# Performance work log

Measured on AMD Instinct MI355X. Metric: run time of the kernel, lower is better.

## Reference

```python
import jax, jax.numpy as jnp
import numpy as np

N, C_IN, H, W = 32, 3, 224, 224
C_OUT, K, STRIDE, PAD = 64, 3, 1, 1


def setup_inputs() -> dict:
    key = jax.random.key(0)
    k1, k2 = jax.random.split(key)
    x = jax.random.normal(k1, (N, C_IN, H, W), dtype=jnp.float32)
    weight = jax.random.normal(k2, (C_OUT, C_IN, K, K), dtype=jnp.float32)
    bias = jnp.zeros((C_OUT,), dtype=jnp.float32)
    return {"x": x, "weight": weight, "bias": bias}


def reference(x, weight, bias):
    # Equivalent to the manual im2col + GEMM: a standard 2D convolution
    # (cross-correlation, as the torch code slides the raw kernel).
    out = jax.lax.conv_general_dilated(
        x, weight,
        window_strides=(STRIDE, STRIDE),
        padding=[(PAD, PAD), (PAD, PAD)],
        dimension_numbers=("NCHW", "OIHW", "NCHW"),
    )
    return out + bias[None, :, None, None]
```

## Files before the change

kernel.cpp:

```cpp
#include <hip/hip_runtime.h>


#define N_IMG 32
#define C_IN 3
#define H_ 224
#define W_ 224
#define C_OUT 64
#define NPIX (H_ * W_)
#define W4 (W_ / 4)
#define STRIPS (NPIX / 4)
#define COB 16

__global__ __launch_bounds__(256) void conv3x3_v2(
    const float* __restrict__ x,
    const float* __restrict__ wgt,
    const float* __restrict__ bias,
    float* __restrict__ out)
{
    const int s  = blockIdx.x * 256 + threadIdx.x;
    const int n  = blockIdx.y;
    const int cb = blockIdx.z * COB;
    const int h  = s / W4;
    const int w4 = (s - h * W4) * 4;

    float win[C_IN][3][6];
    const float* xn = x + (size_t)n * C_IN * NPIX;
#pragma unroll
    for (int ci = 0; ci < C_IN; ++ci) {
#pragma unroll
        for (int r = 0; r < 3; ++r) {
            const int hh = h + r - 1;
            const bool hok = (unsigned)hh < (unsigned)H_;
            const float* row = xn + ci * NPIX + hh * W_;
            if (hok) {
                const float4 m = *reinterpret_cast<const float4*>(row + w4);
                win[ci][r][1] = m.x; win[ci][r][2] = m.y;
                win[ci][r][3] = m.z; win[ci][r][4] = m.w;
                win[ci][r][0] = (w4 > 0)      ? row[w4 - 1] : 0.0f;
                win[ci][r][5] = (w4 + 4 < W_) ? row[w4 + 4] : 0.0f;
            } else {
#pragma unroll
                for (int c = 0; c < 6; ++c) win[ci][r][c] = 0.0f;
            }
        }
    }

    float* outp = out + ((size_t)n * C_OUT + cb) * NPIX + h * W_ + w4;
#pragma unroll
    for (int i = 0; i < COB; ++i) {
        const float* wp = wgt + (size_t)(cb + i) * 27;
        const float b  = bias[cb + i];
        float a0 = b, a1 = b, a2 = b, a3 = b;
#pragma unroll
        for (int ci = 0; ci < C_IN; ++ci)
#pragma unroll
            for (int r = 0; r < 3; ++r)
#pragma unroll
                for (int dc = 0; dc < 3; ++dc) {
                    const float wv = wp[(ci * 3 + r) * 3 + dc];
                    a0 += win[ci][r][0 + dc] * wv;
                    a1 += win[ci][r][1 + dc] * wv;
                    a2 += win[ci][r][2 + dc] * wv;
                    a3 += win[ci][r][3 + dc] * wv;
                }
        float4 o; o.x = a0; o.y = a1; o.z = a2; o.w = a3;
        *reinterpret_cast<float4*>(outp + (size_t)i * NPIX) = o;
    }
}

extern "C" void kernel_launch(void* const* d_in, const int* in_sizes, int n_in,
                              void* d_out, int out_size, void* d_ws, size_t ws_size,
                              hipStream_t stream) {
    const float* x    = (const float*)d_in[0];
    const float* wgt  = (const float*)d_in[1];
    const float* bias = (const float*)d_in[2];
    float* out = (float*)d_out;

    dim3 grid(STRIPS / 256, N_IMG, C_OUT / COB);
    dim3 block(256);
    conv3x3_v2<<<grid, block, 0, stream>>>(x, wgt, bias, out);
}
```

Measured before the change: 467.7 us.

## Restructure conv loop per input channel with 8-channel accumulator groups

```diff
diff --git a/kernel.cpp b/kernel.cpp
--- a/kernel.cpp
+++ b/kernel.cpp
@@ -9,24 +9,32 @@
 #define NPIX (H_ * W_)
 #define W4 (W_ / 4)
 #define STRIPS (NPIX / 4)
-#define COB 16
+#define COG 8
 
-__global__ __launch_bounds__(256) void conv3x3_v2(
+__global__ __launch_bounds__(256, 5) void conv3x3_v3(
     const float* __restrict__ x,
     const float* __restrict__ wgt,
     const float* __restrict__ bias,
     float* __restrict__ out)
 {
     const int s  = blockIdx.x * 256 + threadIdx.x;
-    const int n  = blockIdx.y;
-    const int cb = blockIdx.z * COB;
+    const int cg = blockIdx.y * COG;
+    const int n  = blockIdx.z;
     const int h  = s / W4;
     const int w4 = (s - h * W4) * 4;
 
-    float win[C_IN][3][6];
+    float acc[COG][4];
+#pragma unroll
+    for (int co = 0; co < COG; ++co) {
+        const float b = bias[cg + co];
+        acc[co][0] = b; acc[co][1] = b; acc[co][2] = b; acc[co][3] = b;
+    }
+
     const float* xn = x + (size_t)n * C_IN * NPIX;
-#pragma unroll
+
+#pragma unroll 1
     for (int ci = 0; ci < C_IN; ++ci) {
+        float win[3][6];
 #pragma unroll
         for (int r = 0; r < 3; ++r) {
             const int hh = h + r - 1;
@@ -34,37 +42,40 @@
             const float* row = xn + ci * NPIX + hh * W_;
             if (hok) {
                 const float4 m = *reinterpret_cast<const float4*>(row + w4);
-                win[ci][r][1] = m.x; win[ci][r][2] = m.y;
-                win[ci][r][3] = m.z; win[ci][r][4] = m.w;
-                win[ci][r][0] = (w4 > 0)      ? row[w4 - 1] : 0.0f;
-                win[ci][r][5] = (w4 + 4 < W_) ? row[w4 + 4] : 0.0f;
+                win[r][1] = m.x; win[r][2] = m.y;
+                win[r][3] = m.z; win[r][4] = m.w;
+                win[r][0] = (w4 > 0)      ? row[w4 - 1] : 0.0f;
+                win[r][5] = (w4 + 4 < W_) ? row[w4 + 4] : 0.0f;
             } else {
 #pragma unroll
-                for (int c = 0; c < 6; ++c) win[ci][r][c] = 0.0f;
+                for (int c = 0; c < 6; ++c) win[r][c] = 0.0f;
             }
         }
-    }
 
-    float* outp = out + ((size_t)n * C_OUT + cb) * NPIX + h * W_ + w4;
+        const float* wci = wgt + (size_t)cg * 27 + ci * 9;
 #pragma unroll
-    for (int i = 0; i < COB; ++i) {
-        const float* wp = wgt + (size_t)(cb + i) * 27;
-        const float b  = bias[cb + i];
-        float a0 = b, a1 = b, a2 = b, a3 = b;
-#pragma unroll
-        for (int ci = 0; ci < C_IN; ++ci)
+        for (int co = 0; co < COG; ++co) {
+            const float* wp = wci + (size_t)co * 27;
 #pragma unroll
             for (int r = 0; r < 3; ++r)
 #pragma unroll
                 for (int dc = 0; dc < 3; ++dc) {
-                    const float wv = wp[(ci * 3 + r) * 3 + dc];
-                    a0 += win[ci][r][0 + dc] * wv;
-                    a1 += win[ci][r][1 + dc] * wv;
-                    a2 += win[ci][r][2 + dc] * wv;
-                    a3 += win[ci][r][3 + dc] * wv;
+                    const float wv = wp[r * 3 + dc];
+                    acc[co][0] += win[r][0 + dc] * wv;
+                    acc[co][1] += win[r][1 + dc] * wv;
+                    acc[co][2] += win[r][2 + dc] * wv;
+                    acc[co][3] += win[r][3 + dc] * wv;
                 }
-        float4 o; o.x = a0; o.y = a1; o.z = a2; o.w = a3;
-        *reinterpret_cast<float4*>(outp + (size_t)i * NPIX) = o;
+        }
+    }
+
+    float* outp = out + ((size_t)n * C_OUT + cg) * NPIX + h * W_ + w4;
+#pragma unroll
+    for (int co = 0; co < COG; ++co) {
+        float4 o;
+        o.x = acc[co][0]; o.y = acc[co][1];
+        o.z = acc[co][2]; o.w = acc[co][3];
+        *reinterpret_cast<float4*>(outp + (size_t)co * NPIX) = o;
     }
 }
 
@@ -76,7 +87,7 @@
     const float* bias = (const float*)d_in[2];
     float* out = (float*)d_out;
 
-    dim3 grid(STRIPS / 256, N_IMG, C_OUT / COB);
+    dim3 grid(STRIPS / 256, C_OUT / COG, N_IMG);
     dim3 block(256);
-    conv3x3_v2<<<grid, block, 0, stream>>>(x, wgt, bias, out);
+    conv3x3_v3<<<grid, block, 0, stream>>>(x, wgt, bias, out);
 }
```

Result: no change. 475.6 us (+1.7%).
